# Performance work log

Measured on AMD Instinct MI355X. Metric: run time of the kernel, lower is better.

## Reference

```python
import jax, jax.numpy as jnp
import numpy as np

B, T, D, U = 2, 512, 768, 768


def setup_inputs() -> dict:
    key = jax.random.key(0)
    kx, kv, ku, kw = jax.random.split(key, 4)
    x = jax.random.normal(kx, (B, T, D), dtype=jnp.float32)
    # glorot-ish scaled params
    V_a = jax.random.normal(kv, (U,), dtype=jnp.float32) * (1.0 / np.sqrt(U))
    U_a = jax.random.normal(ku, (D, U), dtype=jnp.float32) * (1.0 / np.sqrt(D))
    b_u = jnp.zeros((U,), dtype=jnp.float32)
    W_a = jax.random.normal(kw, (D, U), dtype=jnp.float32) * (1.0 / np.sqrt(D))
    return {"x": x, "V_a": V_a, "U_a": U_a, "b_u": b_u, "W_a": W_a}


def reference(x, V_a, U_a, b_u, W_a):
    # Bahdanau additive self-attention, fully batched (replaces the per-timestep loop).
    # wx[b,i,u] = x[b,i] @ W_a  (query projection; original recomputed this per step)
    wx = jnp.einsum('bid,du->biu', x, W_a)
    # ux[b,j,u] = x[b,j] @ U_a + b_u  (the _uxpb term)
    ux = jnp.einsum('bjd,du->bju', x, U_a) + b_u
    # e[b,i,j] = V_a . tanh(wx[b,i] + ux[b,j])
    e = jnp.einsum('biju,u->bij', jnp.tanh(wx[:, :, None, :] + ux[:, None, :, :]), V_a)
    # original: exp / sum over keys == softmax over axis j (no mask path)
    at = jax.nn.softmax(e, axis=2)
    # context[b,i,d] = sum_j at[b,i,j] * x[b,j,d]
    return jnp.einsum('bij,bjd->bid', at, x)
```

## Files before the change

kernel.cpp:

```cpp
#include <hip/hip_runtime.h>
#include <hip/hip_bf16.h>

#define BB 2
#define TT 512
#define DD 768
#define UU 768
#define NR (BB*TT)
#define CC 2.8853900817779268f

typedef __attribute__((ext_vector_type(8))) short short8v;
typedef __attribute__((ext_vector_type(4))) float float4v;
typedef __attribute__((ext_vector_type(4))) unsigned short ushort4v;

static __device__ __forceinline__ float fexp2(float x) { return __builtin_amdgcn_exp2f(x); }
static __device__ __forceinline__ float frcp(float x)  { return __builtin_amdgcn_rcpf(x); }
static __device__ __forceinline__ float readlane_f(float v, int l) {
    return __builtin_bit_cast(float, __builtin_amdgcn_readlane(__builtin_bit_cast(unsigned, v), l));
}
static __device__ __forceinline__ unsigned short bf16rn(float f) {
    unsigned u = __builtin_bit_cast(unsigned, f);
    u += 0x7FFFu + ((u >> 16) & 1u);
    return (unsigned short)(u >> 16);
}
static __device__ __forceinline__ float bf16tof(unsigned short h) {
    return __builtin_bit_cast(float, ((unsigned)h) << 16);
}

__global__ __launch_bounds__(256) void prep_split(
    const float* __restrict__ x,
    const float* __restrict__ Wm,
    const float* __restrict__ Um,
    unsigned short* __restrict__ xhi, unsigned short* __restrict__ xlo,
    unsigned short* __restrict__ WThi, unsigned short* __restrict__ WTlo,
    unsigned short* __restrict__ UThi, unsigned short* __restrict__ UTlo)
{
    const int mode = blockIdx.z;
    const int t = threadIdx.x;

    if (mode == 2) {
        const int blk = blockIdx.y * 12 + blockIdx.x;
        const float4* src = (const float4*)x + (size_t)blk * 1024;
        #pragma unroll
        for (int i = 0; i < 4; ++i) {
            const int idx = i * 256 + t;
            const float4 v = src[idx];
            ushort4v h, l;
            h.x = bf16rn(v.x); l.x = bf16rn(v.x - bf16tof(h.x));
            h.y = bf16rn(v.y); l.y = bf16rn(v.y - bf16tof(h.y));
            h.z = bf16rn(v.z); l.z = bf16rn(v.z - bf16tof(h.z));
            h.w = bf16rn(v.w); l.w = bf16rn(v.w - bf16tof(h.w));
            const size_t off = (size_t)blk * 4096 + (size_t)idx * 4;
            *(ushort4v*)(xhi + off) = h;
            *(ushort4v*)(xlo + off) = l;
        }
        return;
    }
    if (blockIdx.y >= 12) return;

    const float* __restrict__ S = (mode == 0) ? Wm : Um;
    unsigned short* __restrict__ Thi = (mode == 0) ? WThi : UThi;
    unsigned short* __restrict__ Tlo = (mode == 0) ? WTlo : UTlo;

    __shared__ float tile[64][65];
    const int d0 = blockIdx.y * 64;
    const int u0 = blockIdx.x * 64;

    #pragma unroll
    for (int i = 0; i < 4; ++i) {
        const int f4 = i * 256 + t;
        const int r  = f4 >> 4;
        const int c4 = f4 & 15;
        const float4 v = *(const float4*)(S + (size_t)(d0 + r) * UU + u0 + c4 * 4);
        tile[r][c4 * 4 + 0] = v.x;
        tile[r][c4 * 4 + 1] = v.y;
        tile[r][c4 * 4 + 2] = v.z;
        tile[r][c4 * 4 + 3] = v.w;
    }
    __syncthreads();
    #pragma unroll
    for (int i = 0; i < 2; ++i) {
        const int cid = i * 256 + t;
        const int ur  = cid >> 3;
        const int kc  = cid & 7;
        short8v H, L;
        #pragma unroll
        for (int j = 0; j < 8; ++j) {
            const float f = tile[kc * 8 + j][ur];
            const unsigned short h = bf16rn(f);
            H[j] = (short)h;
            L[j] = (short)bf16rn(f - bf16tof(h));
        }
        const size_t off = (size_t)(u0 + ur) * DD + d0 + kc * 8;
        *(short8v*)(Thi + off) = H;
        *(short8v*)(Tlo + off) = L;
    }
}

__global__ __launch_bounds__(256) void gemm_mfma(
    const unsigned short* __restrict__ xhi, const unsigned short* __restrict__ xlo,
    const unsigned short* __restrict__ WThi, const unsigned short* __restrict__ WTlo,
    const unsigned short* __restrict__ UThi, const unsigned short* __restrict__ UTlo,
    const float* __restrict__ bu,
    float* __restrict__ EW4,
    float* __restrict__ EUT)
{
    const int mode = blockIdx.z;
    const unsigned short* __restrict__ Ahi = mode ? UThi : WThi;
    const unsigned short* __restrict__ Alo = mode ? UTlo : WTlo;

    __shared__ unsigned short lds[4 * 4096];

    const int tid  = threadIdx.x;
    const int lane = tid & 63;
    const int wid  = tid >> 6;
    const int wm   = wid >> 1, wn = wid & 1;
    const int u0   = blockIdx.y * 64;
    const int r0t  = blockIdx.x * 64;

    const int srow0 = tid >> 3;
    const int srow1 = srow0 + 32;
    const int sc0   = tid & 7;
    const int sw0   = (sc0 ^ (srow0 & 7)) << 3;

    short8v g0, g1, g2, g3, g4, g5, g6, g7;

#define LOADSTEP(K0) { \
    const size_t ka = (size_t)(K0) + sc0 * 8; \
    g0 = *(const short8v*)(Ahi + (size_t)(u0 + srow0) * DD + ka); \
    g1 = *(const short8v*)(Ahi + (size_t)(u0 + srow1) * DD + ka); \
    g2 = *(const short8v*)(Alo + (size_t)(u0 + srow0) * DD + ka); \
    g3 = *(const short8v*)(Alo + (size_t)(u0 + srow1) * DD + ka); \
    g4 = *(const short8v*)(xhi + (size_t)(r0t + srow0) * DD + ka); \
    g5 = *(const short8v*)(xhi + (size_t)(r0t + srow1) * DD + ka); \
    g6 = *(const short8v*)(xlo + (size_t)(r0t + srow0) * DD + ka); \
    g7 = *(const short8v*)(xlo + (size_t)(r0t + srow1) * DD + ka); }

#define WRITESTEP { \
    *(short8v*)&lds[0 * 4096 + srow0 * 64 + sw0] = g0; \
    *(short8v*)&lds[0 * 4096 + srow1 * 64 + sw0] = g1; \
    *(short8v*)&lds[1 * 4096 + srow0 * 64 + sw0] = g2; \
    *(short8v*)&lds[1 * 4096 + srow1 * 64 + sw0] = g3; \
    *(short8v*)&lds[2 * 4096 + srow0 * 64 + sw0] = g4; \
    *(short8v*)&lds[2 * 4096 + srow1 * 64 + sw0] = g5; \
    *(short8v*)&lds[3 * 4096 + srow0 * 64 + sw0] = g6; \
    *(short8v*)&lds[3 * 4096 + srow1 * 64 + sw0] = g7; }

    float4v acc[2][2] = {};

    LOADSTEP(0);
    for (int s = 0; s < 12; ++s) {
        __syncthreads();
        WRITESTEP;
        __syncthreads();
        if (s < 11) LOADSTEP((s + 1) * 64);

        short8v ah[2][2], al[2][2], bh[2][2], bl[2][2];
        #pragma unroll
        for (int f = 0; f < 2; ++f) {
            const int arow = wm * 32 + f * 16 + (lane & 15);
            const int brow = wn * 32 + f * 16 + (lane & 15);
            #pragma unroll
            for (int kk = 0; kk < 2; ++kk) {
                const int ck = kk * 4 + (lane >> 4);
                ah[f][kk] = *(const short8v*)&lds[0 * 4096 + arow * 64 + (((ck ^ (arow & 7))) << 3)];
                al[f][kk] = *(const short8v*)&lds[1 * 4096 + arow * 64 + (((ck ^ (arow & 7))) << 3)];
                bh[f][kk] = *(const short8v*)&lds[2 * 4096 + brow * 64 + (((ck ^ (brow & 7))) << 3)];
                bl[f][kk] = *(const short8v*)&lds[3 * 4096 + brow * 64 + (((ck ^ (brow & 7))) << 3)];
            }
        }
        #pragma unroll
        for (int kk = 0; kk < 2; ++kk)
            #pragma unroll
            for (int m = 0; m < 2; ++m)
                #pragma unroll
                for (int n = 0; n < 2; ++n) {
                    acc[m][n] = __builtin_amdgcn_mfma_f32_16x16x32_bf16(ah[m][kk], bh[n][kk], acc[m][n], 0, 0, 0);
                    acc[m][n] = __builtin_amdgcn_mfma_f32_16x16x32_bf16(ah[m][kk], bl[n][kk], acc[m][n], 0, 0, 0);
                    acc[m][n] = __builtin_amdgcn_mfma_f32_16x16x32_bf16(al[m][kk], bh[n][kk], acc[m][n], 0, 0, 0);
                }
    }

    #pragma unroll
    for (int m = 0; m < 2; ++m) {
        #pragma unroll
        for (int n = 0; n < 2; ++n) {
            const int ub = u0 + wm * 32 + m * 16 + ((lane >> 4) << 2);
            const int r  = r0t + wn * 32 + n * 16 + (lane & 15);
            if (mode == 0) {
                float* dst = EW4 + ((size_t)(r >> 2) * UU + ub) * 4 + (r & 3);
                #pragma unroll
                for (int reg = 0; reg < 4; ++reg)
                    dst[reg * 4] = fexp2(acc[m][n][reg] * CC);
            } else {
                const int b = r >> 9, j = r & 511;
                const float4 bv = *(const float4*)(bu + ub);
                float4v o;
                o[0] = fexp2((acc[m][n][0] + bv.x) * CC);
                o[1] = fexp2((acc[m][n][1] + bv.y) * CC);
                o[2] = fexp2((acc[m][n][2] + bv.z) * CC);
                o[3] = fexp2((acc[m][n][3] + bv.w) * CC);
                *(float4v*)(EUT + (size_t)b * (UU * TT) + (size_t)(ub >> 2) * (TT * 4) + j * 4) = o;
            }
        }
    }
#undef LOADSTEP
#undef WRITESTEP
}

__global__ __launch_bounds__(512) void attn_fused(
    const float* __restrict__ x,
    const float* __restrict__ V_a,
    const float* __restrict__ EW4,
    const float* __restrict__ EUT,
    float* __restrict__ out)
{
    extern __shared__ float smem[];
    float*  part = smem;
    float*  red  = smem;
    float4* tq   = (float4*)(smem + 12288);
    float*  ivh  = smem + 12288 + 3072;

    const int tid  = threadIdx.x;
    const int lane = tid & 63;
    const int w    = tid >> 6;

    const int bid = blockIdx.x;
    const int blk = (bid & 7) * 32 + (bid >> 3);

    const int r0 = blk * 4;
    const int b  = r0 >> 9;

    {
        const float4* __restrict__ ew4q = (const float4*)EW4 + (size_t)blk * UU;
        for (int t = tid; t < UU; t += 512) {
            const float4 s4 = ew4q[t];
            const float rv = frcp(V_a[t]);
            tq[t]  = make_float4(s4.x * rv, s4.y * rv, s4.z * rv, s4.w * rv);
            ivh[t] = rv;
        }
    }
    __syncthreads();

    const float4*  __restrict__ eq  = (const float4*)(EUT + (size_t)b * UU * TT) + tid;
    const float2*  __restrict__ ivp = (const float2*)ivh;

    float acc0 = 0.f, acc1 = 0.f, acc2 = 0.f, acc3 = 0.f;

#define PAIR(E0, E1, p) { \
    const float4 T0 = tq[2 * (p)]; \
    const float4 T1 = tq[2 * (p) + 1]; \
    const float2 IV = ivp[(p)]; \
    { const float da = fmaf((E0), T0.x, IV.x), db = fmaf((E1), T1.x, IV.y); \
      acc0 = fmaf(da + db, frcp(da * db), acc0); } \
    { const float da = fmaf((E0), T0.y, IV.x), db = fmaf((E1), T1.y, IV.y); \
      acc1 = fmaf(da + db, frcp(da * db), acc1); } \
    { const float da = fmaf((E0), T0.z, IV.x), db = fmaf((E1), T1.z, IV.y); \
      acc2 = fmaf(da + db, frcp(da * db), acc2); } \
    { const float da = fmaf((E0), T0.w, IV.x), db = fmaf((E1), T1.w, IV.y); \
      acc3 = fmaf(da + db, frcp(da * db), acc3); } }
#define QUAD(E4, q) { PAIR((E4).x, (E4).y, 2 * (q)); PAIR((E4).z, (E4).w, 2 * (q) + 1); }

    float4 c0 = eq[0 * 512], c1 = eq[1 * 512], c2 = eq[2 * 512], c3 = eq[3 * 512];
    #pragma unroll 1
    for (int c = 0; c < 47; ++c) {
        const int q = 4 * c;
        float4 n0_ = eq[(size_t)(q + 4) * 512];
        float4 n1_ = eq[(size_t)(q + 5) * 512];
        float4 n2_ = eq[(size_t)(q + 6) * 512];
        float4 n3_ = eq[(size_t)(q + 7) * 512];
        QUAD(c0, q); QUAD(c1, q + 1); QUAD(c2, q + 2); QUAD(c3, q + 3);
        c0 = n0_; c1 = n1_; c2 = n2_; c3 = n3_;
    }
    QUAD(c0, 188); QUAD(c1, 189); QUAD(c2, 190); QUAD(c3, 191);

    float m0 = acc0, m1 = acc1, m2 = acc2, m3 = acc3;
    #pragma unroll
    for (int off = 32; off; off >>= 1) {
        m0 = fminf(m0, __shfl_xor(m0, off, 64));
        m1 = fminf(m1, __shfl_xor(m1, off, 64));
        m2 = fminf(m2, __shfl_xor(m2, off, 64));
        m3 = fminf(m3, __shfl_xor(m3, off, 64));
    }
    if (lane == 0) {
        red[0 * 8 + w] = m0; red[1 * 8 + w] = m1;
        red[2 * 8 + w] = m2; red[3 * 8 + w] = m3;
    }
    __syncthreads();
    float M0 = red[0], M1 = red[8], M2 = red[16], M3 = red[24];
    #pragma unroll
    for (int k = 1; k < 8; ++k) {
        M0 = fminf(M0, red[0 * 8 + k]);
        M1 = fminf(M1, red[1 * 8 + k]);
        M2 = fminf(M2, red[2 * 8 + k]);
        M3 = fminf(M3, red[3 * 8 + k]);
    }

    const float p0 = fexp2(CC * (M0 - acc0));
    const float p1 = fexp2(CC * (M1 - acc1));
    const float p2 = fexp2(CC * (M2 - acc2));
    const float p3 = fexp2(CC * (M3 - acc3));
    float s0 = p0, s1 = p1, s2 = p2, s3 = p3;
    #pragma unroll
    for (int off = 32; off; off >>= 1) {
        s0 += __shfl_xor(s0, off, 64);
        s1 += __shfl_xor(s1, off, 64);
        s2 += __shfl_xor(s2, off, 64);
        s3 += __shfl_xor(s3, off, 64);
    }
    __syncthreads();
    if (lane == 0) {
        red[32 + 0 * 8 + w] = s0; red[32 + 1 * 8 + w] = s1;
        red[32 + 2 * 8 + w] = s2; red[32 + 3 * 8 + w] = s3;
    }
    __syncthreads();
    float S0 = red[32], S1 = red[40], S2 = red[48], S3 = red[56];
    #pragma unroll
    for (int k = 1; k < 8; ++k) {
        S0 += red[32 + k];
        S1 += red[40 + k];
        S2 += red[48 + k];
        S3 += red[56 + k];
    }
    const float i0 = frcp(S0), i1 = frcp(S1), i2 = frcp(S2), i3 = frcp(S3);

    const float* __restrict__ xb = x + (size_t)b * TT * DD + (size_t)w * 64 * DD + 4 * lane;
    float4 z4 = {0.f, 0.f, 0.f, 0.f};
    float4 pc00 = z4, pc01 = z4, pc02 = z4;
    float4 pc10 = z4, pc11 = z4, pc12 = z4;
    float4 pc20 = z4, pc21 = z4, pc22 = z4;
    float4 pc30 = z4, pc31 = z4, pc32 = z4;

#define F4(dst, a, xv) { dst.x = fmaf(a, xv.x, dst.x); dst.y = fmaf(a, xv.y, dst.y); \
                         dst.z = fmaf(a, xv.z, dst.z); dst.w = fmaf(a, xv.w, dst.w); }
    #pragma unroll 2
    for (int jj = 0; jj < 64; ++jj) {
        const float a0 = readlane_f(p0, jj);
        const float a1 = readlane_f(p1, jj);
        const float a2 = readlane_f(p2, jj);
        const float a3 = readlane_f(p3, jj);
        const float* xr = xb + (size_t)jj * DD;
        const float4 x0 = *(const float4*)(xr);
        const float4 x1 = *(const float4*)(xr + 256);
        const float4 x2 = *(const float4*)(xr + 512);
        F4(pc00, a0, x0); F4(pc01, a0, x1); F4(pc02, a0, x2);
        F4(pc10, a1, x0); F4(pc11, a1, x1); F4(pc12, a1, x2);
        F4(pc20, a2, x0); F4(pc21, a2, x1); F4(pc22, a2, x2);
        F4(pc30, a3, x0); F4(pc31, a3, x1); F4(pc32, a3, x2);
    }

    __syncthreads();
    {
        float* pw = part + w * 1536 + 4 * lane;
        *(float4*)(pw + 0)    = pc00;
        *(float4*)(pw + 256)  = pc01;
        *(float4*)(pw + 512)  = pc02;
        *(float4*)(pw + 768)  = pc10;
        *(float4*)(pw + 1024) = pc11;
        *(float4*)(pw + 1280) = pc12;
    }
    __syncthreads();
    #pragma unroll
    for (int e = 0; e < 3; ++e) {
        const int idx = e * 512 + tid;
        const int r   = (idx >= 768) ? 1 : 0;
        const int d   = idx - r * 768;
        float ssum = 0.f;
        #pragma unroll
        for (int w2 = 0; w2 < 8; ++w2) ssum += part[w2 * 1536 + r * 768 + d];
        out[(size_t)(r0 + r) * DD + d] = ssum * (r ? i1 : i0);
    }
    __syncthreads();
    {
        float* pw = part + w * 1536 + 4 * lane;
        *(float4*)(pw + 0)    = pc20;
        *(float4*)(pw + 256)  = pc21;
        *(float4*)(pw + 512)  = pc22;
        *(float4*)(pw + 768)  = pc30;
        *(float4*)(pw + 1024) = pc31;
        *(float4*)(pw + 1280) = pc32;
    }
    __syncthreads();
    #pragma unroll
    for (int e = 0; e < 3; ++e) {
        const int idx = e * 512 + tid;
        const int r   = (idx >= 768) ? 1 : 0;
        const int d   = idx - r * 768;
        float ssum = 0.f;
        #pragma unroll
        for (int w2 = 0; w2 < 8; ++w2) ssum += part[w2 * 1536 + r * 768 + d];
        out[(size_t)(r0 + 2 + r) * DD + d] = ssum * (r ? i3 : i2);
    }
}

extern "C" void kernel_launch(void* const* d_in, const int* in_sizes, int n_in,
                              void* d_out, int out_size, void* d_ws, size_t ws_size,
                              hipStream_t stream)
{
    const float* x   = (const float*)d_in[0];
    const float* V_a = (const float*)d_in[1];
    const float* U_a = (const float*)d_in[2];
    const float* b_u = (const float*)d_in[3];
    const float* W_a = (const float*)d_in[4];
    float* out = (float*)d_out;

    float* EW4 = (float*)d_ws;
    float* EUT = EW4 + (size_t)UU * NR;
    unsigned short* xhi  = (unsigned short*)(EUT + (size_t)BB * UU * TT);
    unsigned short* xlo  = xhi + (size_t)NR * DD;
    unsigned short* WThi = xlo + (size_t)NR * DD;
    unsigned short* WTlo = WThi + (size_t)UU * DD;
    unsigned short* UThi = WTlo + (size_t)UU * DD;
    unsigned short* UTlo = UThi + (size_t)UU * DD;

    hipLaunchKernelGGL(prep_split, dim3(12, 16, 3), dim3(256), 0, stream,
                       x, W_a, U_a, xhi, xlo, WThi, WTlo, UThi, UTlo);

    hipLaunchKernelGGL(gemm_mfma, dim3(16, 12, 2), dim3(256), 0, stream,
                       xhi, xlo, WThi, WTlo, UThi, UTlo, b_u, EW4, EUT);

    const int ldsB = (12288 + 3072 + 768) * sizeof(float);
    hipLaunchKernelGGL(attn_fused, dim3(NR / 4), dim3(512), ldsB, stream,
                       x, V_a, EW4, EUT, out);
}
```

Measured before the change: 79.32 us.

## Split fused attention kernel into U-split score kernel and softmax-PV kernel

The fused attention kernel is split in two. The first kernel computes partial score sums over half of the U dimension per block, which doubles the grid to 512 blocks. The second kernel adds the two partials and then runs the softmax and the PV product. This is meant to raise parallelism and occupancy for the dominant score loop (256 blocks is close to the CU count). The cost is an extra launch and a partial-score round trip through global memory.

```diff
diff --git a/kernel.cpp b/kernel.cpp
--- a/kernel.cpp
+++ b/kernel.cpp
@@ -207,42 +207,35 @@
 #undef WRITESTEP
 }
 
-__global__ __launch_bounds__(512) void attn_fused(
-    const float* __restrict__ x,
+__global__ __launch_bounds__(512) void attn_e(
     const float* __restrict__ V_a,
     const float* __restrict__ EW4,
     const float* __restrict__ EUT,
-    float* __restrict__ out)
+    float* __restrict__ pacc)
 {
-    extern __shared__ float smem[];
-    float*  part = smem;
-    float*  red  = smem;
-    float4* tq   = (float4*)(smem + 12288);
-    float*  ivh  = smem + 12288 + 3072;
-
-    const int tid  = threadIdx.x;
-    const int lane = tid & 63;
-    const int w    = tid >> 6;
+    __shared__ float4 tq[384];
+    __shared__ float  ivh[384];
+
+    const int tid = threadIdx.x;
 
     const int bid = blockIdx.x;
-    const int blk = (bid & 7) * 32 + (bid >> 3);
-
-    const int r0 = blk * 4;
-    const int b  = r0 >> 9;
-
-    {
-        const float4* __restrict__ ew4q = (const float4*)EW4 + (size_t)blk * UU;
-        for (int t = tid; t < UU; t += 512) {
-            const float4 s4 = ew4q[t];
-            const float rv = frcp(V_a[t]);
-            tq[t]  = make_float4(s4.x * rv, s4.y * rv, s4.z * rv, s4.w * rv);
-            ivh[t] = rv;
-        }
-    }
-    __syncthreads();
-
-    const float4*  __restrict__ eq  = (const float4*)(EUT + (size_t)b * UU * TT) + tid;
-    const float2*  __restrict__ ivp = (const float2*)ivh;
+    const int lin = (bid & 7) * 64 + (bid >> 3);
+    const int rg  = lin >> 1;
+    const int uh  = lin & 1;
+    const int b   = rg >> 7;
+    const int ub0 = uh * 384;
+
+    if (tid < 384) {
+        const float4 s4 = ((const float4*)EW4)[(size_t)rg * UU + ub0 + tid];
+        const float rv = frcp(V_a[ub0 + tid]);
+        tq[tid]  = make_float4(s4.x * rv, s4.y * rv, s4.z * rv, s4.w * rv);
+        ivh[tid] = rv;
+    }
+    __syncthreads();
+
+    const float4* __restrict__ eq =
+        (const float4*)(EUT + (size_t)b * UU * TT) + (size_t)(uh * 96) * 512 + tid;
+    const float2* __restrict__ ivp = (const float2*)ivh;
 
     float acc0 = 0.f, acc1 = 0.f, acc2 = 0.f, acc3 = 0.f;
 
@@ -262,7 +255,7 @@
 
     float4 c0 = eq[0 * 512], c1 = eq[1 * 512], c2 = eq[2 * 512], c3 = eq[3 * 512];
     #pragma unroll 1
-    for (int c = 0; c < 47; ++c) {
+    for (int c = 0; c < 23; ++c) {
         const int q = 4 * c;
         float4 n0_ = eq[(size_t)(q + 4) * 512];
         float4 n1_ = eq[(size_t)(q + 5) * 512];
@@ -271,7 +264,37 @@
         QUAD(c0, q); QUAD(c1, q + 1); QUAD(c2, q + 2); QUAD(c3, q + 3);
         c0 = n0_; c1 = n1_; c2 = n2_; c3 = n3_;
     }
-    QUAD(c0, 188); QUAD(c1, 189); QUAD(c2, 190); QUAD(c3, 191);
+    QUAD(c0, 92); QUAD(c1, 93); QUAD(c2, 94); QUAD(c3, 95);
+#undef PAIR
+#undef QUAD
+
+    *(float4*)(pacc + ((size_t)lin * 512 + tid) * 4) =
+        make_float4(acc0, acc1, acc2, acc3);
+}
+
+__global__ __launch_bounds__(512) void attn_pv(
+    const float* __restrict__ x,
+    const float* __restrict__ pacc,
+    float* __restrict__ out)
+{
+    extern __shared__ float smem[];
+    float* part = smem;
+    float* red  = smem;
+
+    const int tid  = threadIdx.x;
+    const int lane = tid & 63;
+    const int w    = tid >> 6;
+
+    const int bid = blockIdx.x;
+    const int blk = (bid & 7) * 32 + (bid >> 3);
+
+    const int r0 = blk * 4;
+    const int b  = r0 >> 9;
+
+    const float4 A0 = *(const float4*)(pacc + ((size_t)(blk * 2 + 0) * 512 + tid) * 4);
+    const float4 A1 = *(const float4*)(pacc + ((size_t)(blk * 2 + 1) * 512 + tid) * 4);
+    float acc0 = A0.x + A1.x, acc1 = A0.y + A1.y;
+    float acc2 = A0.z + A1.z, acc3 = A0.w + A1.w;
 
     float m0 = acc0, m1 = acc1, m2 = acc2, m3 = acc3;
     #pragma unroll
@@ -347,6 +370,7 @@
         F4(pc20, a2, x0); F4(pc21, a2, x1); F4(pc22, a2, x2);
         F4(pc30, a3, x0); F4(pc31, a3, x1); F4(pc32, a3, x2);
     }
+#undef F4
 
     __syncthreads();
     {
@@ -411,6 +435,7 @@
     unsigned short* WTlo = WThi + (size_t)UU * DD;
     unsigned short* UThi = WTlo + (size_t)UU * DD;
     unsigned short* UTlo = UThi + (size_t)UU * DD;
+    float* pacc = (float*)(UTlo + (size_t)UU * DD);
 
     hipLaunchKernelGGL(prep_split, dim3(12, 16, 3), dim3(256), 0, stream,
                        x, W_a, U_a, xhi, xlo, WThi, WTlo, UThi, UTlo);
@@ -418,7 +443,10 @@
     hipLaunchKernelGGL(gemm_mfma, dim3(16, 12, 2), dim3(256), 0, stream,
                        xhi, xlo, WThi, WTlo, UThi, UTlo, b_u, EW4, EUT);
 
-    const int ldsB = (12288 + 3072 + 768) * sizeof(float);
-    hipLaunchKernelGGL(attn_fused, dim3(NR / 4), dim3(512), ldsB, stream,
-                       x, V_a, EW4, EUT, out);
-}
+    hipLaunchKernelGGL(attn_e, dim3(512), dim3(512), 0, stream,
+                       V_a, EW4, EUT, pacc);
+
+    const int ldsB = 12288 * sizeof(float);
+    hipLaunchKernelGGL(attn_pv, dim3(256), dim3(512), ldsB, stream,
+                       x, pacc, out);
+}
```

Result: slower. 82.18 us (+3.6%).
